# Kernel optimization log

Hardware: AMD Instinct MI355X
Metric: run time of the kernel (lower is better)

Reference implementation:

```python
import jax, jax.numpy as jnp
import numpy as np

STEP, LEAK = 16, 32
KS = STEP + LEAK          # kernel_size = 48
FODEP = KS                # forced depression window
SYNAPSES, NEURONS = 64, 256
IC, OC = 1, 10
DENSE = 0.5
THETA = DENSE * SYNAPSES * IC   # 32.0
BIAS = 0.5
BATCH, TIME = 16, 512


def setup_inputs() -> dict:
    key = jax.random.key(0)
    k1, k2 = jax.random.split(key)
    # binary input spikes, density 0.2
    input_spikes = (jax.random.uniform(k1, (BATCH, IC, SYNAPSES, TIME)) < 0.2).astype(jnp.float32)
    # weight ~ Exponential(rate=1/w_init=2).sample().clip(0,1), mean 0.5
    u = jax.random.uniform(k2, (OC * NEURONS, IC * SYNAPSES), minval=1e-6, maxval=1.0)
    weight = jnp.clip(-0.5 * jnp.log(u), 0.0, 1.0)
    return {"input_spikes": input_spikes, "weight": weight}


def _step_fire_leak_kernel(weight):
    # kernel[o, i, t] = max(0, min(t/step, -(t - w*step)/leak + w)), flipped on t
    t = jnp.arange(KS, dtype=weight.dtype)
    t_spike = t / STEP                                        # rising edge
    t_leak = -(t - weight[..., None] * STEP) / LEAK + weight[..., None]  # decaying edge
    kernel = jnp.maximum(jnp.zeros((), weight.dtype), jnp.minimum(t_spike, t_leak))
    return kernel[..., ::-1]


def _forward(input_spikes, weight):
    B, C, S, T = input_spikes.shape
    x = input_spikes.reshape(B, C * S, T)
    kernel = _step_fire_leak_kernel(weight)                   # [OC*N, IC*S, KS]
    # conv1d with padding = kernel_size on both sides -> T' = T + KS + 1
    pot = jax.lax.conv_general_dilated(
        x, kernel, window_strides=(1,), padding=[(KS, KS)],
        dimension_numbers=("NCH", "OIH", "NCH"))
    Tp = pot.shape[-1]
    pot = pot.reshape(B, OC, NEURONS, Tp) + BIAS * THETA      # unsupervised bias path

    # winner-takes-all scan over time with per-(batch, neuron) depression counter
    pot_t = pot.transpose(3, 0, 2, 1)                         # [T', B, N, OC]
    dep0 = jnp.zeros((B, NEURONS, OC), jnp.int32)

    def step_fn(dep, p):
        masked = jnp.where(dep == 0, p, jnp.zeros((), p.dtype))
        winner = jnp.argmax(masked, axis=-1)                  # [B, N]
        wpot = jnp.take_along_axis(masked, winner[..., None], axis=-1)[..., 0]
        spike = (wpot > THETA).astype(p.dtype)                # [B, N]
        w_t = jax.nn.one_hot(winner, OC, dtype=p.dtype) * spike[..., None]
        dep = jnp.clip(dep + spike.astype(jnp.int32)[..., None] * FODEP - 1, 0, FODEP - 1)
        return dep, w_t

    _, winners = jax.lax.scan(step_fn, dep0, pot_t)           # [T', B, N, OC]
    return winners.transpose(1, 3, 2, 0)                      # [B, OC, N, T'] float


def reference(input_spikes, weight):
    return _forward(input_spikes, weight)
```

## Files before the change

kernel.cpp:

```cpp
#include <hip/hip_runtime.h>

#define B_   16
#define OC_  10
#define N_   256
#define O_   2560
#define S_   64
#define T_   512
#define KS_  48
#define TP_  561
#define TT   24
#define WROW 72

#define NOC   160
#define XROWS 624

#define SCH    16
#define CPITCH 572

using i32x4 = __attribute__((ext_vector_type(4))) int;

__global__ void prep_all(const float* __restrict__ x, const float* __restrict__ w,
                         unsigned char* __restrict__ xb, signed char* __restrict__ Bg) {
    if (blockIdx.x < 512) {
#pragma unroll
        for (int it = 0; it < 4; ++it) {
            int idx = blockIdx.x * 256 + threadIdx.x + it * 131072;
            int t = idx & 511;
            int bi = idx >> 9;
            int i = bi & 63, b = bi >> 6;
            xb[((size_t)(b * 512 + t) << 6) + i] = (x[idx] != 0.0f) ? 1 : 0;
        }
    } else {
        int base = (blockIdx.x - 512) * 256 + threadIdx.x;
#pragma unroll
        for (int it = 0; it < 16; ++it) {
            int idx = base + it * 491520;
            int i = idx & 63;
            int oj = idx >> 6;
            int j = oj % KS_, o = oj / KS_;
            float wv = w[(o << 6) + i];
            float rise = (float)j * 0.0625f;
            float leak = -((float)j - wv * 16.0f) * 0.03125f + wv;
            float kv   = fmaxf(0.0f, fminf(rise, leak));
            int q  = (int)lrintf(kv * 4194304.0f);
            int d0 = ((q + 128) & 255) - 128;
            int q1 = (q - d0) >> 8;
            int d1 = ((q1 + 128) & 255) - 128;
            int d2 = (q1 - d1) >> 8;
            int oc = o >> 4, ol = o & 15;
            int jm = j & 15, jh = j >> 4;
            int pos = jm * 3 + jh;
            size_t bse = (((size_t)(oc * KS_ + pos) * 48) + ol) * 64 + i;
            Bg[bse]            = (signed char)d0;
            Bg[bse + 16 * 64]  = (signed char)d1;
            Bg[bse + 32 * 64]  = (signed char)d2;
        }
    }
}

__global__ __launch_bounds__(256, 2) void gemm_i8(
    const unsigned char* __restrict__ xb,
    const signed char*  __restrict__ Bg,
    float* __restrict__ pot)
{
    __shared__ __align__(16) unsigned char xT[XROWS * 64];

    const int tid  = threadIdx.x;
    const int lane = tid & 63;
    const int wave = tid >> 6;
    const int oc = blockIdx.x;
    const int b  = blockIdx.y;
    const int lrow = lane & 15;
    const int quad = lane >> 4;
    const int tw = wave * 144;

    const signed char* Bgb = Bg + (size_t)oc * (KS_ * 48 * 64)
                           + lrow * 64 + quad * 16;

    for (int z = tid; z < 112 * 4; z += 256) {
        int zi = z >> 2, p = z & 3;
        int r = (zi < 49) ? zi : (561 + zi - 49);
        *(i32x4*)(xT + r * 64 + p * 16) = (i32x4){0, 0, 0, 0};
    }
    const unsigned char* xbb = xb + ((size_t)b << 15);
    for (int q = tid; q < 2048; q += 256) {
        i32x4 v = *(const i32x4*)(xbb + q * 16);
        int t = q >> 2, p = q & 3;
        int r = 49 + t;
        *(i32x4*)(xT + r * 64 + ((p ^ ((r >> 1) & 3)) << 4)) = v;
    }

    i32x4 acc[9][3];
#pragma unroll
    for (int mi = 0; mi < 9; ++mi)
#pragma unroll
        for (int f = 0; f < 3; ++f)
            acc[mi][f] = (i32x4){0, 0, 0, 0};

    i32x4 af[11], bfA[9], bfB[9];

#pragma unroll
    for (int jh = 0; jh < 3; ++jh)
#pragma unroll
        for (int f = 0; f < 3; ++f)
            bfA[jh * 3 + f] = *(const i32x4*)(Bgb + jh * 3072 + f * 1024);

    __syncthreads();

    {
        const int rb0 = tw + 16 + lrow;
        const int ca0 = ((quad ^ ((rb0 >> 1) & 3)) << 4);
#pragma unroll
        for (int k = 0; k < 11; ++k)
            af[k] = *(const i32x4*)(xT + (rb0 + k * 16) * 64 + ca0);
    }

#define MF(bfC, mi, jh, f)                                                    \
    acc[mi][f] = __builtin_amdgcn_mfma_i32_16x16x64_i8(                       \
        af[(mi) + 2 - (jh)], bfC[(jh) * 3 + (f)], acc[mi][f], 0, 0, 0)

#define PAIR(bfC, m0)                                                         \
    MF(bfC, m0, 0, 0); MF(bfC, m0, 0, 1); MF(bfC, m0, 0, 2);                  \
    MF(bfC, (m0)+1, 0, 0); MF(bfC, (m0)+1, 0, 1); MF(bfC, (m0)+1, 0, 2);      \
    MF(bfC, m0, 1, 0); MF(bfC, m0, 1, 1); MF(bfC, m0, 1, 2);                  \
    MF(bfC, (m0)+1, 1, 0); MF(bfC, (m0)+1, 1, 1); MF(bfC, (m0)+1, 1, 2);      \
    MF(bfC, m0, 2, 0); MF(bfC, m0, 2, 1); MF(bfC, m0, 2, 2);                  \
    MF(bfC, (m0)+1, 2, 0); MF(bfC, (m0)+1, 2, 1); MF(bfC, (m0)+1, 2, 2);

#define PAIR9(bfC)                                                            \
    MF(bfC, 8, 0, 0); MF(bfC, 8, 0, 1); MF(bfC, 8, 0, 2);                     \
    MF(bfC, 8, 1, 0); MF(bfC, 8, 1, 1); MF(bfC, 8, 1, 2);                     \
    MF(bfC, 8, 2, 0); MF(bfC, 8, 2, 1); MF(bfC, 8, 2, 2);

#define LDA_(row) (*(const i32x4*)(xT + (row) * 64 + coffN))
#define LDB_(jh, f) (*(const i32x4*)(Bgb + (tn3 + (jh)) * 3072 + (f) * 1024))

#define TLOC(T, bfC, bfN) {                                                   \
        const int rbn   = tw + 16 - ((T) + 1) + lrow;    \
        const int coffN = ((quad ^ ((rbn >> 1) & 3)) << 4);                   \
        const int tn3   = (((T) + 1) & 15) * 3;         \
        __builtin_amdgcn_s_setprio(1);                                        \
        PAIR(bfC, 0)                                                          \
        af[0] = LDA_(rbn);        af[1] = LDA_(rbn + 16);                     \
        bfN[0] = LDB_(0, 0); bfN[1] = LDB_(0, 1); bfN[2] = LDB_(0, 2);        \
        PAIR(bfC, 2)                                                          \
        af[2] = LDA_(rbn + 32);   af[3] = LDA_(rbn + 48);                     \
        bfN[3] = LDB_(1, 0); bfN[4] = LDB_(1, 1); bfN[5] = LDB_(1, 2);        \
        PAIR(bfC, 4)                                                          \
        af[4] = LDA_(rbn + 64);   af[5] = LDA_(rbn + 80);                     \
        bfN[6] = LDB_(2, 0); bfN[7] = LDB_(2, 1); bfN[8] = LDB_(2, 2);        \
        PAIR(bfC, 6)                                                          \
        af[6] = LDA_(rbn + 96);   af[7] = LDA_(rbn + 112);                    \
        PAIR9(bfC)                                                            \
        af[8] = LDA_(rbn + 128);  af[9] = LDA_(rbn + 144);                    \
        af[10] = LDA_(rbn + 160);                                             \
        __builtin_amdgcn_s_setprio(0);                                        \
    }

    for (int tp = 0; tp < 8; ++tp) {
        TLOC(2 * tp,     bfA, bfB)
        TLOC(2 * tp + 1, bfB, bfA)
    }

#undef MF
#undef PAIR
#undef PAIR9
#undef LDA_
#undef LDB_
#undef TLOC

    const size_t potb = (size_t)b * TP_;
#pragma unroll
    for (int mi = 0; mi < 9; ++mi) {
#pragma unroll
        for (int r = 0; r < 4; ++r) {
            int t = tw + mi * 16 + quad * 4 + r;
            if (t < TP_) {
                double pq = ((double)acc[mi][0][r]
                           + 256.0   * (double)acc[mi][1][r]
                           + 65536.0 * (double)acc[mi][2][r])
                          * (1.0 / 4194304.0);
                pot[(potb + t) * O_ + oc * 16 + lrow] = (float)pq;
            }
        }
    }
}

__global__ __launch_bounds__(1024) void scan_fused(
    const float* __restrict__ pot,
    float* __restrict__ out)
{
    __shared__ unsigned char codeW[SCH * CPITCH];
    __shared__ unsigned char ocW[SCH * CPITCH];

    const int tid = threadIdx.x;
    const int nc = blockIdx.x;
    const int b  = blockIdx.y;
    const int n0 = nc * SCH;

    for (int pair = tid; pair < TP_ * SCH; pair += 1024) {
        int t = pair >> 4, nl = pair & 15;
        const float* p = pot + ((size_t)(b * TP_ + t)) * O_ + n0 + nl;
        float best = p[0]; int bo = 0;
#pragma unroll
        for (int ch = 1; ch < OC_; ++ch) {
            float v = p[ch * N_];
            if (v > best) { best = v; bo = ch; }
        }
        codeW[nl * CPITCH + t] =
            ((best + 16.0f) > 32.0f) ? (unsigned char)(bo + 1) : (unsigned char)0;
        ocW[nl * CPITCH + t] = 0;
    }
    __syncthreads();

    if (tid < SCH) {
        const unsigned char* c = &codeW[tid * CPITCH];
        unsigned char* o = &ocW[tid * CPITCH];
        int t = 0;
        while (t < TP_) {
            unsigned char buf[KS_];
#pragma unroll
            for (int k = 0; k < KS_; ++k) {
                int tt = t + k;
                buf[k] = (tt < TP_) ? c[tt] : (unsigned char)0;
            }
            int adv = KS_;
#pragma unroll
            for (int k = 0; k < KS_; ++k) {
                if (buf[k]) { o[t + k] = buf[k]; adv = k + KS_; break; }
            }
            t += adv;
        }
    }
    __syncthreads();

    float* ob = out + (((size_t)b * OC_) * N_ + n0) * TP_;
    for (int idx = tid; idx < OC_ * SCH * TP_; idx += 1024) {
        int r = idx / TP_;
        int t = idx - r * TP_;
        int ch = r >> 4, nl = r & 15;
        float v = (ocW[nl * CPITCH + t] == (unsigned char)(ch + 1)) ? 1.0f : 0.0f;
        ob[((size_t)ch * N_ + nl) * TP_ + t] = v;
    }
}

__global__ void transpose_w(const float* __restrict__ w, float* __restrict__ wT) {
    int idx = blockIdx.x * 256 + threadIdx.x;
    if (idx >= O_ * S_) return;
    int o = idx >> 6, i = idx & 63;
    wT[i * O_ + o] = w[idx];
}

__global__ __launch_bounds__(256) void conv_kernel(
    const float* __restrict__ x, const float* __restrict__ wT,
    float* __restrict__ pot)
{
    const int b  = blockIdx.y;
    const int t0 = blockIdx.z * TT;
    const int o  = blockIdx.x * 256 + threadIdx.x;

    __shared__ __align__(16) float xsh[S_][WROW];
    for (int idx = threadIdx.x; idx < S_ * WROW; idx += 256) {
        int i = idx / WROW, m = idx - i * WROW;
        int t = t0 - KS_ + m;
        float v = 0.0f;
        if (t >= 0 && t < T_) v = x[(b * S_ + i) * T_ + t];
        xsh[i][m] = v;
    }
    __syncthreads();

    float acch[TT], accl[TT];
#pragma unroll
    for (int tl = 0; tl < TT; ++tl) { acch[tl] = 0.0f; accl[tl] = 0.0f; }

    for (int i = 0; i < S_; ++i) {
        float xw[WROW];
#pragma unroll
        for (int w4 = 0; w4 < WROW / 4; ++w4) {
            const float4 v = *reinterpret_cast<const float4*>(&xsh[i][w4 * 4]);
            xw[w4 * 4 + 0] = v.x; xw[w4 * 4 + 1] = v.y;
            xw[w4 * 4 + 2] = v.z; xw[w4 * 4 + 3] = v.w;
        }
        const float wv = wT[i * O_ + o];
#pragma unroll
        for (int j = 1; j < KS_; ++j) {
            float rise = (float)j * 0.0625f;
            float leak = -((float)j - wv * 16.0f) * 0.03125f + wv;
            float kv   = fmaxf(0.0f, fminf(rise, leak));
            float khi  = rintf(kv * 4096.0f) * 2.44140625e-4f;
            float klo  = kv - khi;
#pragma unroll
            for (int tl = 0; tl < TT; ++tl) {
                float xv = xw[tl + (KS_ - 1) - j];
                acch[tl] = fmaf(xv, khi, acch[tl]);
                accl[tl] = fmaf(xv, klo, accl[tl]);
            }
        }
    }
#pragma unroll
    for (int tl = 0; tl < TT; ++tl) {
        int t = t0 + tl;
        if (t < TP_) pot[((size_t)b * TP_ + t) * O_ + o] = acch[tl] + accl[tl];
    }
}

__global__ void scan_prep(const float* __restrict__ pot, unsigned char* __restrict__ code) {
    int idx = blockIdx.x * 256 + threadIdx.x;
    if (idx >= B_ * TP_ * N_) return;
    int n  = idx & (N_ - 1);
    int bt = idx >> 8;
    const float* p = pot + (size_t)bt * O_ + n;
    float best = p[0]; int bo = 0;
#pragma unroll
    for (int oc = 1; oc < OC_; ++oc) {
        float v = p[oc * N_];
        if (v > best) { best = v; bo = oc; }
    }
    code[idx] = ((best + 16.0f) > 32.0f) ? (unsigned char)(bo + 1) : (unsigned char)0;
}

__global__ void scan_run(const unsigned char* __restrict__ code, float* __restrict__ out) {
    int idx = blockIdx.x * 256 + threadIdx.x;
    if (idx >= B_ * N_) return;
    int b = idx >> 8, n = idx & 255;
    const unsigned char* c = code + (size_t)b * TP_ * N_ + n;
    int t = 0;
    while (t < TP_) {
        unsigned char buf[KS_];
#pragma unroll
        for (int k = 0; k < KS_; ++k) {
            int tt = t + k;
            buf[k] = (tt < TP_) ? c[(size_t)tt * N_] : (unsigned char)0;
        }
        int adv = KS_;
#pragma unroll
        for (int k = 0; k < KS_; ++k) {
            if (buf[k]) {
                out[(((size_t)b * OC_ + (buf[k] - 1)) * N_ + n) * TP_ + (t + k)] = 1.0f;
                adv = k + KS_;
                break;
            }
        }
        t += adv;
    }
}

extern "C" void kernel_launch(void* const* d_in, const int* in_sizes, int n_in,
                              void* d_out, int out_size, void* d_ws, size_t ws_size,
                              hipStream_t stream) {
    const float* x = (const float*)d_in[0];
    const float* w = (const float*)d_in[1];
    float* out = (float*)d_out;

    char* ws = (char*)d_ws;
    const size_t szX = (size_t)B_ * T_ * S_;
    const size_t szB = (size_t)NOC * KS_ * 48 * 64;
    const size_t szP = (size_t)B_ * TP_ * O_ * 4;
    const size_t szC = (size_t)B_ * TP_ * N_;
    const size_t need = szX + szB + szP + szC;

    if (ws_size >= need) {
        unsigned char* xb  = (unsigned char*)ws;
        signed char* Bg    = (signed char*)(ws + szX);
        float* pot         = (float*)(ws + szX + szB);

        prep_all<<<2432, 256, 0, stream>>>(x, w, xb, Bg);
        gemm_i8<<<dim3(NOC, B_), 256, 0, stream>>>(xb, Bg, pot);
        scan_fused<<<dim3(N_ / SCH, B_), 1024, 0, stream>>>(pot, out);
    } else {
        size_t pot_bytes  = (size_t)B_ * TP_ * O_ * sizeof(float);
        size_t code_bytes = (size_t)B_ * TP_ * N_;
        float* pot = (float*)ws;
        unsigned char* code = (unsigned char*)(ws + pot_bytes);
        float* wT = (float*)(ws + pot_bytes + code_bytes);

        hipMemsetAsync(d_out, 0, (size_t)out_size * sizeof(float), stream);
        transpose_w<<<(O_ * S_ + 255) / 256, 256, 0, stream>>>(w, wT);
        conv_kernel<<<dim3(O_ / 256, B_, (TP_ + TT - 1) / TT), 256, 0, stream>>>(x, wT, pot);
        scan_prep<<<(B_ * TP_ * N_ + 255) / 256, 256, 0, stream>>>(pot, code);
        scan_run<<<(B_ * N_ + 255) / 256, 256, 0, stream>>>(code, out);
    }
}
```

Baseline: 256.0 us.

## Split GEMM across six waves with single B buffer; parallelize WTA scan via ballot

The int8 MFMA conv kernel goes from 4 waves covering 144 time rows each to 6 waves covering 96 rows each. This shrinks the accumulator and A-fragment register sets and drops the double-buffered B fragments in favour of a single buffer that is reloaded in place, which should allow more resident waves. The scan stage now runs one wave per neuron and uses a 64-lane ballot with count-trailing-zeros to find the next spike, replacing a serial 48-element loop run by a single thread. The risks are that B loads are now less overlapped with MFMA work, and that there are more blocks' worth of waves competing for the same SIMDs.

```diff
diff --git a/kernel.cpp b/kernel.cpp
--- a/kernel.cpp
+++ b/kernel.cpp
@@ -58,7 +58,7 @@
     }
 }
 
-__global__ __launch_bounds__(256, 2) void gemm_i8(
+__global__ __launch_bounds__(384, 3) void gemm_i8(
     const unsigned char* __restrict__ xb,
     const signed char*  __restrict__ Bg,
     float* __restrict__ pot)
@@ -72,38 +72,38 @@
     const int b  = blockIdx.y;
     const int lrow = lane & 15;
     const int quad = lane >> 4;
-    const int tw = wave * 144;
+    const int tw = wave * 96;
 
     const signed char* Bgb = Bg + (size_t)oc * (KS_ * 48 * 64)
                            + lrow * 64 + quad * 16;
 
-    for (int z = tid; z < 112 * 4; z += 256) {
+    for (int z = tid; z < 112 * 4; z += 384) {
         int zi = z >> 2, p = z & 3;
         int r = (zi < 49) ? zi : (561 + zi - 49);
         *(i32x4*)(xT + r * 64 + p * 16) = (i32x4){0, 0, 0, 0};
     }
     const unsigned char* xbb = xb + ((size_t)b << 15);
-    for (int q = tid; q < 2048; q += 256) {
+    for (int q = tid; q < 2048; q += 384) {
         i32x4 v = *(const i32x4*)(xbb + q * 16);
         int t = q >> 2, p = q & 3;
         int r = 49 + t;
         *(i32x4*)(xT + r * 64 + ((p ^ ((r >> 1) & 3)) << 4)) = v;
     }
 
-    i32x4 acc[9][3];
-#pragma unroll
-    for (int mi = 0; mi < 9; ++mi)
+    i32x4 acc[6][3];
+#pragma unroll
+    for (int mi = 0; mi < 6; ++mi)
 #pragma unroll
         for (int f = 0; f < 3; ++f)
             acc[mi][f] = (i32x4){0, 0, 0, 0};
 
-    i32x4 af[11], bfA[9], bfB[9];
+    i32x4 af[8], bf[9];
 
 #pragma unroll
     for (int jh = 0; jh < 3; ++jh)
 #pragma unroll
         for (int f = 0; f < 3; ++f)
-            bfA[jh * 3 + f] = *(const i32x4*)(Bgb + jh * 3072 + f * 1024);
+            bf[jh * 3 + f] = *(const i32x4*)(Bgb + jh * 3072 + f * 1024);
 
     __syncthreads();
 
@@ -111,67 +111,59 @@
         const int rb0 = tw + 16 + lrow;
         const int ca0 = ((quad ^ ((rb0 >> 1) & 3)) << 4);
 #pragma unroll
-        for (int k = 0; k < 11; ++k)
+        for (int k = 0; k < 8; ++k)
             af[k] = *(const i32x4*)(xT + (rb0 + k * 16) * 64 + ca0);
     }
 
-#define MF(bfC, mi, jh, f)                                                    \
+#define MF(mi, jh, f)                                                         \
     acc[mi][f] = __builtin_amdgcn_mfma_i32_16x16x64_i8(                       \
-        af[(mi) + 2 - (jh)], bfC[(jh) * 3 + (f)], acc[mi][f], 0, 0, 0)
-
-#define PAIR(bfC, m0)                                                         \
-    MF(bfC, m0, 0, 0); MF(bfC, m0, 0, 1); MF(bfC, m0, 0, 2);                  \
-    MF(bfC, (m0)+1, 0, 0); MF(bfC, (m0)+1, 0, 1); MF(bfC, (m0)+1, 0, 2);      \
-    MF(bfC, m0, 1, 0); MF(bfC, m0, 1, 1); MF(bfC, m0, 1, 2);                  \
-    MF(bfC, (m0)+1, 1, 0); MF(bfC, (m0)+1, 1, 1); MF(bfC, (m0)+1, 1, 2);      \
-    MF(bfC, m0, 2, 0); MF(bfC, m0, 2, 1); MF(bfC, m0, 2, 2);                  \
-    MF(bfC, (m0)+1, 2, 0); MF(bfC, (m0)+1, 2, 1); MF(bfC, (m0)+1, 2, 2);
-
-#define PAIR9(bfC)                                                            \
-    MF(bfC, 8, 0, 0); MF(bfC, 8, 0, 1); MF(bfC, 8, 0, 2);                     \
-    MF(bfC, 8, 1, 0); MF(bfC, 8, 1, 1); MF(bfC, 8, 1, 2);                     \
-    MF(bfC, 8, 2, 0); MF(bfC, 8, 2, 1); MF(bfC, 8, 2, 2);
+        af[(mi) + 2 - (jh)], bf[(jh) * 3 + (f)], acc[mi][f], 0, 0, 0)
 
 #define LDA_(row) (*(const i32x4*)(xT + (row) * 64 + coffN))
 #define LDB_(jh, f) (*(const i32x4*)(Bgb + (tn3 + (jh)) * 3072 + (f) * 1024))
 
-#define TLOC(T, bfC, bfN) {                                                   \
-        const int rbn   = tw + 16 - ((T) + 1) + lrow;    \
-        const int coffN = ((quad ^ ((rbn >> 1) & 3)) << 4);                   \
-        const int tn3   = (((T) + 1) & 15) * 3;         \
-        __builtin_amdgcn_s_setprio(1);                                        \
-        PAIR(bfC, 0)                                                          \
-        af[0] = LDA_(rbn);        af[1] = LDA_(rbn + 16);                     \
-        bfN[0] = LDB_(0, 0); bfN[1] = LDB_(0, 1); bfN[2] = LDB_(0, 2);        \
-        PAIR(bfC, 2)                                                          \
-        af[2] = LDA_(rbn + 32);   af[3] = LDA_(rbn + 48);                     \
-        bfN[3] = LDB_(1, 0); bfN[4] = LDB_(1, 1); bfN[5] = LDB_(1, 2);        \
-        PAIR(bfC, 4)                                                          \
-        af[4] = LDA_(rbn + 64);   af[5] = LDA_(rbn + 80);                     \
-        bfN[6] = LDB_(2, 0); bfN[7] = LDB_(2, 1); bfN[8] = LDB_(2, 2);        \
-        PAIR(bfC, 6)                                                          \
-        af[6] = LDA_(rbn + 96);   af[7] = LDA_(rbn + 112);                    \
-        PAIR9(bfC)                                                            \
-        af[8] = LDA_(rbn + 128);  af[9] = LDA_(rbn + 144);                    \
-        af[10] = LDA_(rbn + 160);                                             \
-        __builtin_amdgcn_s_setprio(0);                                        \
-    }
-
-    for (int tp = 0; tp < 8; ++tp) {
-        TLOC(2 * tp,     bfA, bfB)
-        TLOC(2 * tp + 1, bfB, bfA)
+#pragma unroll
+    for (int t = 0; t < 16; ++t) {
+        const int tn  = (t + 1) & 15;
+        const int rbn = tw + 16 - tn + lrow;
+        const int coffN = ((quad ^ ((rbn >> 1) & 3)) << 4);
+        const int tn3 = tn * 3;
+
+        __builtin_amdgcn_s_setprio(1);
+        MF(0,0,0); MF(0,0,1); MF(0,0,2);  MF(1,0,0); MF(1,0,1); MF(1,0,2);
+        MF(2,0,0); MF(2,0,1); MF(2,0,2);  MF(3,0,0); MF(3,0,1); MF(3,0,2);
+        MF(4,0,0); MF(4,0,1); MF(4,0,2);  MF(5,0,0); MF(5,0,1); MF(5,0,2);
+        __builtin_amdgcn_s_setprio(0);
+        bf[0] = LDB_(0, 0); bf[1] = LDB_(0, 1); bf[2] = LDB_(0, 2);
+
+        __builtin_amdgcn_s_setprio(1);
+        MF(0,1,0); MF(0,1,1); MF(0,1,2);  MF(1,1,0); MF(1,1,1); MF(1,1,2);
+        MF(2,1,0); MF(2,1,1); MF(2,1,2);
+        af[7] = LDA_(rbn + 112);
+        MF(3,1,0); MF(3,1,1); MF(3,1,2);  MF(4,1,0); MF(4,1,1); MF(4,1,2);
+        MF(5,1,0); MF(5,1,1); MF(5,1,2);
+        __builtin_amdgcn_s_setprio(0);
+        bf[3] = LDB_(1, 0); bf[4] = LDB_(1, 1); bf[5] = LDB_(1, 2);
+
+        __builtin_amdgcn_s_setprio(1);
+        af[6] = LDA_(rbn + 96);
+        MF(0,2,0); MF(0,2,1); MF(0,2,2);  af[0] = LDA_(rbn);
+        MF(1,2,0); MF(1,2,1); MF(1,2,2);  af[1] = LDA_(rbn + 16);
+        MF(2,2,0); MF(2,2,1); MF(2,2,2);  af[2] = LDA_(rbn + 32);
+        MF(3,2,0); MF(3,2,1); MF(3,2,2);  af[3] = LDA_(rbn + 48);
+        MF(4,2,0); MF(4,2,1); MF(4,2,2);  af[4] = LDA_(rbn + 64);
+        MF(5,2,0); MF(5,2,1); MF(5,2,2);  af[5] = LDA_(rbn + 80);
+        __builtin_amdgcn_s_setprio(0);
+        bf[6] = LDB_(2, 0); bf[7] = LDB_(2, 1); bf[8] = LDB_(2, 2);
     }
 
 #undef MF
-#undef PAIR
-#undef PAIR9
 #undef LDA_
 #undef LDB_
-#undef TLOC
 
     const size_t potb = (size_t)b * TP_;
 #pragma unroll
-    for (int mi = 0; mi < 9; ++mi) {
+    for (int mi = 0; mi < 6; ++mi) {
 #pragma unroll
         for (int r = 0; r < 4; ++r) {
             int t = tw + mi * 16 + quad * 4 + r;
@@ -213,23 +205,20 @@
     }
     __syncthreads();
 
-    if (tid < SCH) {
-        const unsigned char* c = &codeW[tid * CPITCH];
-        unsigned char* o = &ocW[tid * CPITCH];
+    {
+        const int wv = tid >> 6;
+        const int ln = tid & 63;
+        const unsigned char* c = &codeW[wv * CPITCH];
+        unsigned char* o = &ocW[wv * CPITCH];
         int t = 0;
         while (t < TP_) {
-            unsigned char buf[KS_];
-#pragma unroll
-            for (int k = 0; k < KS_; ++k) {
-                int tt = t + k;
-                buf[k] = (tt < TP_) ? c[tt] : (unsigned char)0;
-            }
-            int adv = KS_;
-#pragma unroll
-            for (int k = 0; k < KS_; ++k) {
-                if (buf[k]) { o[t + k] = buf[k]; adv = k + KS_; break; }
-            }
-            t += adv;
+            int tt = t + ln;
+            unsigned char v = (tt < TP_) ? c[tt] : (unsigned char)0;
+            unsigned long long mask = __ballot(v != 0);
+            if (mask == 0ULL) { t += 64; continue; }
+            int k = (int)__builtin_ctzll(mask);
+            if (ln == k) o[t + k] = v;
+            t += k + KS_;
         }
     }
     __syncthreads();
@@ -365,7 +354,7 @@
         float* pot         = (float*)(ws + szX + szB);
 
         prep_all<<<2432, 256, 0, stream>>>(x, w, xb, Bg);
-        gemm_i8<<<dim3(NOC, B_), 256, 0, stream>>>(xb, Bg, pot);
+        gemm_i8<<<dim3(NOC, B_), 384, 0, stream>>>(xb, Bg, pot);
         scan_fused<<<dim3(N_ / SCH, B_), 1024, 0, stream>>>(pot, out);
     } else {
         size_t pot_bytes  = (size_t)B_ * TP_ * O_ * sizeof(float);
```

Result: slower. 287.2 us (+12.2%).
